# Performance work log

Hardware: AMD Instinct MI355X
Metric: run time of the kernel (lower is better)

## Reference

```python
import jax, jax.numpy as jnp
import numpy as np

N, E, F_IN, HID, G, HEADS = 50000, 300000, 128, 256, 1000, 1
NUM_GC, ALPHA = 5, 0.5
EPS_LN = 1e-5
EPS_BN = 1e-5


def _layer_norm(h, g, b):
    m = h.mean(-1, keepdims=True)
    v = jnp.mean((h - m) ** 2, axis=-1, keepdims=True)
    return (h - m) * jax.lax.rsqrt(v + EPS_LN) * g + b


def _l2_normalize_rows(h):
    # F.normalize(h, dim=1)
    n = jnp.sqrt(jnp.sum(h * h, axis=1, keepdims=True))
    return h / jnp.maximum(n, 1e-12)


def full_attention_conv(qs, ks, vs):
    # qs:[N,H,M] ks:[L,H,M] vs:[L,H,D]; global (Frobenius) norm as in torch.norm(p=2)
    qs = qs / jnp.linalg.norm(qs)
    ks = ks / jnp.linalg.norm(ks)
    n = qs.shape[0]
    kvs = jnp.einsum('lhm,lhd->hmd', ks, vs)                 # [H,M,D]
    attn_num = jnp.einsum('nhm,hmd->nhd', qs, kvs) + n * vs  # [N,H,D]
    ks_sum = ks.sum(axis=0)                                  # [H,M]
    norm = jnp.einsum('nhm,hm->nh', qs, ks_sum)[..., None] + n
    return attn_num / norm                                   # [N,H,D]


def setup_inputs() -> dict:
    key = jax.random.key(0)
    ks = jax.random.split(key, 24)
    f32 = jnp.float32

    def lin(k, fan_in, shape):
        return jax.random.normal(k, shape, f32) / np.sqrt(fan_in)

    inp = {}
    inp['x'] = jax.random.normal(ks[0], (N, F_IN), f32)
    inp['edge_index'] = jax.random.randint(ks[1], (2, E), 0, N)
    inp['batch'] = jnp.sort(jax.random.randint(ks[2], (N,), 0, G))
    inp['beta'] = 1
    # TransConv params
    inp['fc_W'] = lin(ks[3], F_IN, (F_IN, HID)); inp['fc_b'] = jnp.zeros((HID,), f32)
    inp['ln0_g'] = jnp.ones((HID,), f32); inp['ln0_b'] = jnp.zeros((HID,), f32)
    inp['Wq'] = lin(ks[4], HID, (HID, HID * HEADS)); inp['bq'] = jnp.zeros((HID * HEADS,), f32)
    inp['Wk'] = lin(ks[5], HID, (HID, HID * HEADS)); inp['bk'] = jnp.zeros((HID * HEADS,), f32)
    inp['Wv'] = lin(ks[6], HID, (HID, HID * HEADS)); inp['bv'] = jnp.zeros((HID * HEADS,), f32)
    inp['ln1_g'] = jnp.ones((HID,), f32); inp['ln1_b'] = jnp.zeros((HID,), f32)
    # GCN stack params
    inp['gcn_W0'] = lin(ks[7], F_IN, (F_IN, HID)); inp['gcn_b0'] = jnp.zeros((HID,), f32)
    inp['gcn_W'] = jnp.stack([lin(ks[8 + i], HID, (HID, HID)) for i in range(NUM_GC - 1)])
    inp['gcn_b'] = jnp.zeros((NUM_GC - 1, HID), f32)
    inp['bn_g'] = jnp.ones((NUM_GC, HID), f32); inp['bn_b'] = jnp.zeros((NUM_GC, HID), f32)
    inp['bn_mean'] = jnp.zeros((NUM_GC, HID), f32); inp['bn_var'] = jnp.ones((NUM_GC, HID), f32)
    return inp


def reference(x, edge_index, batch, beta, fc_W, fc_b, ln0_g, ln0_b,
              Wq, bq, Wk, bk, Wv, bv, ln1_g, ln1_b,
              gcn_W0, gcn_b0, gcn_W, gcn_b, bn_g, bn_b, bn_mean, bn_var):
    n = x.shape[0]
    # ---- TransConv branch (eval mode: dropout = identity) ----
    h = jax.nn.relu(_layer_norm(x @ fc_W + fc_b, ln0_g, ln0_b))
    qs = (h @ Wq + bq).reshape(n, HEADS, HID)
    kk = (h @ Wk + bk).reshape(n, HEADS, HID)
    vv = (h @ Wv + bv).reshape(n, HEADS, HID)
    attn = full_attention_conv(qs, kk, vv).mean(axis=1)      # [N,HID]
    h1 = ALPHA * attn + (1.0 - ALPHA) * h                    # residual
    h1 = jax.nn.relu(_layer_norm(h1, ln1_g, ln1_b))
    x_trans = _l2_normalize_rows(h1)
    # ---- GCN stack ----
    src, dst = edge_index[0], edge_index[1]
    loop = jnp.arange(n)
    src_f = jnp.concatenate([src, loop])
    dst_f = jnp.concatenate([dst, loop])
    deg = jax.ops.segment_sum(jnp.ones_like(src_f, dtype=x.dtype), dst_f, num_segments=n)
    dinv = jax.lax.rsqrt(deg)  # deg >= 1 due to self loops
    enorm = (dinv[src_f] * dinv[dst_f])[:, None]             # [E+N,1]
    g = x
    for i in range(NUM_GC):
        W = gcn_W0 if i == 0 else gcn_W[i - 1]
        b = gcn_b0 if i == 0 else gcn_b[i - 1]
        gw = g @ W
        g = jax.ops.segment_sum(gw[src_f] * enorm, dst_f, num_segments=n) + b
        g = (g - bn_mean[i]) * jax.lax.rsqrt(bn_var[i] + EPS_BN) * bn_g[i] + bn_b[i]
        if i != NUM_GC - 1:
            g = jax.nn.relu(g)
    g = _l2_normalize_rows(g)
    xpool = jax.ops.segment_sum(g, batch, num_segments=G)    # global_add_pool
    return (xpool, g, x_trans)
```

## Files before the change

kernel.cpp:

```cpp
#include <hip/hip_runtime.h>
#include <stdint.h>

#define NN 50000
#define NEDGE 300000
#define FIN 128
#define HID 256
#define NG 1000
#define NLAYER 5

typedef __bf16 bf16x8 __attribute__((ext_vector_type(8)));
typedef float f32x4 __attribute__((ext_vector_type(4)));

__device__ __forceinline__ float us2f(unsigned short u){
  union{ unsigned int i; float f; } c; c.i = ((unsigned int)u) << 16; return c.f;
}
__device__ __forceinline__ unsigned short f2us(float f){
  union{ float f; unsigned int i; } c; c.f = f;
  unsigned int r = c.i + 0x7fff + ((c.i >> 16) & 1);
  return (unsigned short)(r >> 16);
}

__device__ __forceinline__ void gload16(const void* g, void* l){
  __builtin_amdgcn_global_load_lds((__attribute__((address_space(1))) void*)g,
                                   (__attribute__((address_space(3))) void*)l, 16, 0, 0);
}

__device__ __forceinline__ void fma8(float* a, uint4 u, float w){
  a[0] += w * us2f((unsigned short)(u.x & 0xffff));
  a[1] += w * us2f((unsigned short)(u.x >> 16));
  a[2] += w * us2f((unsigned short)(u.y & 0xffff));
  a[3] += w * us2f((unsigned short)(u.y >> 16));
  a[4] += w * us2f((unsigned short)(u.z & 0xffff));
  a[5] += w * us2f((unsigned short)(u.z >> 16));
  a[6] += w * us2f((unsigned short)(u.w & 0xffff));
  a[7] += w * us2f((unsigned short)(u.w >> 16));
}

template<int K, int EPI>
__global__ void gemm_epi(const unsigned short* __restrict__ A,
                         const unsigned short* __restrict__ Wt,
                         const float* __restrict__ bias,
                         const float* __restrict__ p1,
                         const float* __restrict__ p2,
                         const unsigned short* __restrict__ hres,
                         void* __restrict__ outv, int nrows)
{
  __shared__ __align__(16) char smem[40960];
  unsigned short* Alds = (unsigned short*)smem;
  unsigned short* Wlds = (unsigned short*)(smem + 8192);
  const int t = threadIdx.x;
  const int lane = t & 63, w = t >> 6;
  const int r0 = blockIdx.x * 64;

  const int ccl = (t & 3) ^ ((t >> 3) & 3);
  int arow = r0 + (t >> 2); if (arow > nrows - 1) arow = nrows - 1;
  const unsigned short* aSrc = A + (size_t)arow * K + ccl * 8;
  const unsigned short* wSrc[4];
#pragma unroll
  for (int i = 0; i < 4; ++i){
    int c = i * 64 + (t >> 2);
    wSrc[i] = Wt + (size_t)c * K + ccl * 8;
  }

  f32x4 acc[4][4] = {};
  const int lg = lane >> 4, lr = lane & 15;

  for (int k0 = 0; k0 < K; k0 += 64){
    gload16(aSrc + k0,      smem + t * 16);
    gload16(aSrc + k0 + 32, smem + 4096 + t * 16);
#pragma unroll
    for (int i = 0; i < 4; ++i){
      gload16(wSrc[i] + k0,      smem + 8192  + (i * 256 + t) * 16);
      gload16(wSrc[i] + k0 + 32, smem + 24576 + (i * 256 + t) * 16);
    }
    __syncthreads();

#pragma unroll
    for (int kk = 0; kk < 2; ++kk){
      const unsigned short* Ak = Alds + kk * 2048;
      const unsigned short* Wk = Wlds + kk * 8192;
      bf16x8 af[4], bfr[4];
#pragma unroll
      for (int mi = 0; mi < 4; ++mi){
        int r = mi * 16 + lr;
        int cp = lg ^ ((r >> 1) & 3);
        af[mi] = *(const bf16x8*)(Ak + (r * 4 + cp) * 8);
      }
#pragma unroll
      for (int ni = 0; ni < 4; ++ni){
        int c = w * 64 + ni * 16 + lr;
        int cp = lg ^ ((c >> 1) & 3);
        bfr[ni] = *(const bf16x8*)(Wk + (c * 4 + cp) * 8);
      }
#pragma unroll
      for (int mi = 0; mi < 4; ++mi)
#pragma unroll
        for (int ni = 0; ni < 4; ++ni)
          acc[mi][ni] = __builtin_amdgcn_mfma_f32_16x16x32_bf16(af[mi], bfr[ni], acc[mi][ni], 0, 0, 0);
    }
    __syncthreads();
  }

  float g1[4], g2[4], bc[4];
#pragma unroll
  for (int ni = 0; ni < 4; ++ni){
    int c = w * 64 + ni * 16 + lr;
    g1[ni] = p1[c]; g2[ni] = p2[c];
    if (EPI <= 2) bc[ni] = bias[c];
  }

  float* redS = (float*)smem;
  float* redQ = redS + 256;
  float* meanr = redQ + 256;
  float* rstdr = meanr + 64;
  float* invr  = rstdr + 64;

  if (EPI == 1 || EPI == 2){
#pragma unroll
    for (int mi = 0; mi < 4; ++mi)
#pragma unroll
      for (int ni = 0; ni < 4; ++ni)
#pragma unroll
        for (int e = 0; e < 4; ++e){
          float v = acc[mi][ni][e] + bc[ni];
          if (EPI == 2){
            int gr = r0 + mi * 16 + lg * 4 + e; if (gr > nrows - 1) gr = nrows - 1;
            int c = w * 64 + ni * 16 + lr;
            v = 0.5f * v + 0.5f * us2f(hres[(size_t)gr * 256 + c]);
          }
          acc[mi][ni][e] = v;
        }
    float ps[4][4], pq[4][4];
#pragma unroll
    for (int mi = 0; mi < 4; ++mi)
#pragma unroll
      for (int e = 0; e < 4; ++e){
        float s = 0.f, q = 0.f;
#pragma unroll
        for (int ni = 0; ni < 4; ++ni){ float v = acc[mi][ni][e]; s += v; q += v * v; }
        ps[mi][e] = s; pq[mi][e] = q;
      }
#pragma unroll
    for (int m = 1; m <= 8; m <<= 1)
#pragma unroll
      for (int mi = 0; mi < 4; ++mi)
#pragma unroll
        for (int e = 0; e < 4; ++e){
          ps[mi][e] += __shfl_xor(ps[mi][e], m);
          pq[mi][e] += __shfl_xor(pq[mi][e], m);
        }
    if (lr == 0){
#pragma unroll
      for (int mi = 0; mi < 4; ++mi)
#pragma unroll
        for (int e = 0; e < 4; ++e){
          int row = mi * 16 + lg * 4 + e;
          redS[w * 64 + row] = ps[mi][e];
          redQ[w * 64 + row] = pq[mi][e];
        }
    }
    __syncthreads();
    if (t < 64){
      float S = redS[t] + redS[64 + t] + redS[128 + t] + redS[192 + t];
      float Q = redQ[t] + redQ[64 + t] + redQ[128 + t] + redQ[192 + t];
      float mean = S * (1.f / 256.f);
      float var = Q * (1.f / 256.f) - mean * mean;
      meanr[t] = mean; rstdr[t] = rsqrtf(var + 1e-5f);
    }
    __syncthreads();
#pragma unroll
    for (int mi = 0; mi < 4; ++mi)
#pragma unroll
      for (int e = 0; e < 4; ++e){
        int row = mi * 16 + lg * 4 + e;
        float mean = meanr[row], rstd = rstdr[row];
#pragma unroll
        for (int ni = 0; ni < 4; ++ni){
          float y = (acc[mi][ni][e] - mean) * rstd * g1[ni] + g2[ni];
          acc[mi][ni][e] = fmaxf(y, 0.f);
        }
      }
  } else {
#pragma unroll
    for (int mi = 0; mi < 4; ++mi)
#pragma unroll
      for (int ni = 0; ni < 4; ++ni)
#pragma unroll
        for (int e = 0; e < 4; ++e){
          float y = acc[mi][ni][e] * g1[ni] + g2[ni];
          if (EPI == 3) y = fmaxf(y, 0.f);
          acc[mi][ni][e] = y;
        }
  }

  if (EPI == 1 || EPI == 3){
    unsigned short* out = (unsigned short*)outv;
#pragma unroll
    for (int mi = 0; mi < 4; ++mi)
#pragma unroll
      for (int e = 0; e < 4; ++e){
        int gr = r0 + mi * 16 + lg * 4 + e;
        if (gr < nrows){
          unsigned short* orow = out + (size_t)gr * 256 + w * 64 + lr;
#pragma unroll
          for (int ni = 0; ni < 4; ++ni)
            orow[ni * 16] = f2us(acc[mi][ni][e]);
        }
      }
  } else {
    float ps[4][4];
#pragma unroll
    for (int mi = 0; mi < 4; ++mi)
#pragma unroll
      for (int e = 0; e < 4; ++e){
        float s = 0.f;
#pragma unroll
        for (int ni = 0; ni < 4; ++ni){ float v = acc[mi][ni][e]; s += v * v; }
        ps[mi][e] = s;
      }
#pragma unroll
    for (int m = 1; m <= 8; m <<= 1)
#pragma unroll
      for (int mi = 0; mi < 4; ++mi)
#pragma unroll
        for (int e = 0; e < 4; ++e)
          ps[mi][e] += __shfl_xor(ps[mi][e], m);
    __syncthreads();
    if (lr == 0){
#pragma unroll
      for (int mi = 0; mi < 4; ++mi)
#pragma unroll
        for (int e = 0; e < 4; ++e)
          redS[w * 64 + mi * 16 + lg * 4 + e] = ps[mi][e];
    }
    __syncthreads();
    if (t < 64){
      float S = redS[t] + redS[64 + t] + redS[128 + t] + redS[192 + t];
      invr[t] = 1.f / fmaxf(sqrtf(S), 1e-12f);
    }
    __syncthreads();
    float* out = (float*)outv;
#pragma unroll
    for (int mi = 0; mi < 4; ++mi)
#pragma unroll
      for (int e = 0; e < 4; ++e){
        int row = mi * 16 + lg * 4 + e;
        int gr = r0 + row;
        float inv = invr[row];
        if (gr < nrows){
          float* orow = out + (size_t)gr * 256 + w * 64 + lr;
#pragma unroll
          for (int ni = 0; ni < 4; ++ni)
            orow[ni * 16] = acc[mi][ni][e] * inv;
        }
      }
  }
}

#define PB_CVT 3125
#define PB_WP  112
#define PB_BN  NLAYER
#define PB_GB  196
#define PB_DC  1172
#define PB_TOTAL (PB_CVT + PB_WP + PB_BN + PB_GB + PB_DC)

__global__ void k_pre(const float* __restrict__ x, unsigned short* __restrict__ xb,
                      const float* __restrict__ fcW, const float* __restrict__ Wv,
                      const float* __restrict__ gW0, const float* __restrict__ gW,
                      unsigned short* __restrict__ fcWt, unsigned short* __restrict__ WvT,
                      unsigned short* __restrict__ g0T, unsigned short* __restrict__ gWT,
                      const float* __restrict__ gb0, const float* __restrict__ gb,
                      const float* __restrict__ bng, const float* __restrict__ bnb,
                      const float* __restrict__ bnm, const float* __restrict__ bnv,
                      float* __restrict__ bnscale, float* __restrict__ bnshift,
                      const int* __restrict__ batch, int* __restrict__ gstart,
                      const int* __restrict__ ei, int* __restrict__ deg)
{
  __shared__ unsigned short tile[64][65];
  int b = blockIdx.x, t = threadIdx.x;
  if (b < PB_CVT){
    int i = b * 256 + t;
    const float4* sp = (const float4*)x + (size_t)i * 2;
    float4 a = sp[0], bb = sp[1];
    ushort4 u0, u1;
    u0.x = f2us(a.x); u0.y = f2us(a.y); u0.z = f2us(a.z); u0.w = f2us(a.w);
    u1.x = f2us(bb.x); u1.y = f2us(bb.y); u1.z = f2us(bb.z); u1.w = f2us(bb.w);
    ushort4* dp = (ushort4*)xb + (size_t)i * 2;
    dp[0] = u0; dp[1] = u1;
    return;
  }
  b -= PB_CVT;
  if (b < PB_WP){
    int which = b >> 4, r = b & 15;
    const float* src; unsigned short* dst; int K;
    if (which == 0){ src = fcW; dst = fcWt; K = FIN; }
    else if (which == 1){ src = Wv; dst = WvT; K = 256; }
    else if (which == 2){ src = gW0; dst = g0T; K = FIN; }
    else { src = gW + (size_t)(which - 3) * 65536; dst = gWT + (size_t)(which - 3) * 65536; K = 256; }
    int bx = (r & 3) * 64; if (bx >= K) return;
    int by = (r >> 2) * 64;
#pragma unroll
    for (int j = 0; j < 16; ++j){
      int idx = j * 256 + t;
      int rr = idx >> 6, cc = idx & 63;
      tile[rr][cc] = f2us(src[(size_t)(bx + rr) * 256 + by + cc]);
    }
    __syncthreads();
#pragma unroll
    for (int j = 0; j < 16; ++j){
      int idx = j * 256 + t;
      int rr = idx >> 6, cc = idx & 63;
      dst[(size_t)(by + rr) * K + bx + cc] = tile[cc][rr];
    }
    return;
  }
  b -= PB_WP;
  if (b < PB_BN){
    int i = b * 256 + t;
    float bias = (b == 0) ? gb0[t] : gb[(b - 1) * 256 + t];
    float sc = bng[i] * rsqrtf(bnv[i] + 1e-5f);
    bnscale[i] = sc;
    bnshift[i] = (bias - bnm[i]) * sc + bnb[i];
    return;
  }
  b -= PB_BN;
  if (b < PB_GB){
    int i = b * 256 + t;
    if (i >= NN) return;
    int bc = batch[i];
    int bp = (i == 0) ? -1 : batch[i - 1];
    for (int g = bp + 1; g <= bc; ++g) gstart[g] = i;
    if (i == NN - 1)
      for (int g = bc + 1; g <= NG; ++g) gstart[g] = NN;
    return;
  }
  b -= PB_GB;
  {
    int e = b * 256 + t;
    if (e < NEDGE) atomicAdd(&deg[ei[NEDGE + e]], 1);
  }
}

__global__ void k_scan_part(const int* __restrict__ deg, int* rp, int* bsum){
  __shared__ int sh[256];
  int t = threadIdx.x, i = blockIdx.x * 256 + t;
  int v = (i < NN) ? deg[i] + 1 : 0;
  sh[t] = v; __syncthreads();
  for (int off = 1; off < 256; off <<= 1){
    int x = (t >= off) ? sh[t - off] : 0;
    __syncthreads(); sh[t] += x; __syncthreads();
  }
  if (i < NN) rp[i] = sh[t] - v;
  if (t == 255) bsum[blockIdx.x] = sh[255];
}
__global__ void k_scan_sums(int* rp, int* bsum, int nb){
  __shared__ int sh[256];
  int t = threadIdx.x;
  int v = (t < nb) ? bsum[t] : 0;
  sh[t] = v; __syncthreads();
  for (int off = 1; off < 256; off <<= 1){
    int x = (t >= off) ? sh[t - off] : 0;
    __syncthreads(); sh[t] += x; __syncthreads();
  }
  if (t < nb) bsum[t] = sh[t] - v;
  if (t == 0) rp[NN] = sh[255];
}
__global__ void k_scan_add(int* rp, const int* __restrict__ bsum, const int* __restrict__ deg,
                           int* fill, float* dinv){
  int i = blockIdx.x * 256 + threadIdx.x;
  if (i < NN){
    int r = rp[i] + bsum[i >> 8];
    rp[i] = r; fill[i] = r;
    dinv[i] = rsqrtf((float)(deg[i] + 1));
  }
}

__global__ void k_fill(const int* __restrict__ ei, int* __restrict__ fill,
                       int* __restrict__ colx, float* __restrict__ ew,
                       const float* __restrict__ dinv)
{
  int e = blockIdx.x * 256 + threadIdx.x;
  if (e < NEDGE){
    int s = ei[e], d = ei[NEDGE + e];
    int p = atomicAdd(&fill[d], 1);
    colx[p] = s; ew[p] = dinv[s] * dinv[d];
  } else if (e < NEDGE + NN){
    int i = e - NEDGE;
    int p = atomicAdd(&fill[i], 1);
    float di = dinv[i];
    colx[p] = i; ew[p] = di * di;
  }
}

template<int NC>
__global__ void __launch_bounds__(256) k_aggregate(
    const unsigned short* __restrict__ gsrc, const int* __restrict__ rp,
    const int* __restrict__ colx, const float* __restrict__ ew,
    unsigned short* __restrict__ gout)
{
  constexpr int LG = (NC == 256) ? 5 : 4;
  int tid = blockIdx.x * 256 + threadIdx.x;
  int nd = tid >> LG;
  if (nd >= NN) return;
  int c0 = (tid & ((1 << LG) - 1)) * 8;
  const unsigned short* base = gsrc + c0;
  int jb = rp[nd], je = rp[nd + 1];
  float a0[8] = {}, a1[8] = {};
  int j = jb;
  for (; j + 2 <= je; j += 2){
    int s0 = colx[j], s1 = colx[j + 1];
    float w0 = ew[j], w1 = ew[j + 1];
    uint4 u0 = *(const uint4*)(base + (size_t)s0 * NC);
    uint4 u1 = *(const uint4*)(base + (size_t)s1 * NC);
    fma8(a0, u0, w0);
    fma8(a1, u1, w1);
  }
  if (j < je){
    uint4 u = *(const uint4*)(base + (size_t)colx[j] * NC);
    fma8(a0, u, ew[j]);
  }
  uint4 pk;
  pk.x = (unsigned int)f2us(a0[0] + a1[0]) | ((unsigned int)f2us(a0[1] + a1[1]) << 16);
  pk.y = (unsigned int)f2us(a0[2] + a1[2]) | ((unsigned int)f2us(a0[3] + a1[3]) << 16);
  pk.z = (unsigned int)f2us(a0[4] + a1[4]) | ((unsigned int)f2us(a0[5] + a1[5]) << 16);
  pk.w = (unsigned int)f2us(a0[6] + a1[6]) | ((unsigned int)f2us(a0[7] + a1[7]) << 16);
  *(uint4*)(gout + (size_t)nd * NC + c0) = pk;
}

__global__ void k_pool(const float* __restrict__ out1, const int* __restrict__ gstart,
                       float* __restrict__ out0)
{
  int g = blockIdx.x, c = threadIdx.x;
  int js = gstart[g], je = gstart[g + 1];
  float acc = 0.f;
  int r = js;
  for (; r + 4 <= je; r += 4){
    float a = out1[(size_t)r * 256 + c];
    float b = out1[(size_t)(r + 1) * 256 + c];
    float d = out1[(size_t)(r + 2) * 256 + c];
    float e = out1[(size_t)(r + 3) * 256 + c];
    acc += (a + b) + (d + e);
  }
  for (; r < je; ++r) acc += out1[(size_t)r * 256 + c];
  out0[(size_t)g * 256 + c] = acc;
}

extern "C" void kernel_launch(void* const* d_in, const int* in_sizes, int n_in,
                              void* d_out, int out_size, void* d_ws, size_t ws_size,
                              hipStream_t stream)
{
  const float* x    = (const float*)d_in[0];
  const int*  ei    = (const int*)d_in[1];
  const int*  batch = (const int*)d_in[2];
  const float* fcW  = (const float*)d_in[4];
  const float* fcb  = (const float*)d_in[5];
  const float* ln0g = (const float*)d_in[6];
  const float* ln0b = (const float*)d_in[7];
  const float* Wv   = (const float*)d_in[12];
  const float* bv   = (const float*)d_in[13];
  const float* ln1g = (const float*)d_in[14];
  const float* ln1b = (const float*)d_in[15];
  const float* gW0  = (const float*)d_in[16];
  const float* gb0  = (const float*)d_in[17];
  const float* gW   = (const float*)d_in[18];
  const float* gb   = (const float*)d_in[19];
  const float* bng  = (const float*)d_in[20];
  const float* bnb  = (const float*)d_in[21];
  const float* bnm  = (const float*)d_in[22];
  const float* bnv  = (const float*)d_in[23];

  char* ws = (char*)d_ws;
  unsigned short* xb   = (unsigned short*)(ws);
  unsigned short* hb   = (unsigned short*)(ws + 12800000);
  unsigned short* ga   = (unsigned short*)(ws + 38400000);
  unsigned short* fcWt = (unsigned short*)(ws + 64000000);
  unsigned short* WvT  = (unsigned short*)(ws + 64065536);
  unsigned short* g0T  = (unsigned short*)(ws + 64196608);
  unsigned short* gWT  = (unsigned short*)(ws + 64262144);
  float* bnscale       = (float*)(ws + 64786432);
  float* bnshift       = (float*)(ws + 64791552);
  int*   deg           = (int*)(ws + 64796672);
  int*   rp            = (int*)(ws + 64996672);
  int*   fill          = (int*)(ws + 65196736);
  float* dinv          = (float*)(ws + 65396736);
  int*   colx          = (int*)(ws + 65596736);
  float* ew            = (float*)(ws + 66996736);
  int*   bsum          = (int*)(ws + 68396736);
  int*   gstart        = (int*)(ws + 68397760);

  float* out0 = (float*)d_out;
  float* out1 = out0 + NG * 256;
  float* out2 = out1 + NN * 256;

  hipMemsetAsync(deg, 0, NN * sizeof(int), stream);
  k_pre<<<PB_TOTAL, 256, 0, stream>>>(x, xb, fcW, Wv, gW0, gW, fcWt, WvT, g0T, gWT,
                                      gb0, gb, bng, bnb, bnm, bnv, bnscale, bnshift,
                                      batch, gstart, ei, deg);
  k_scan_part<<<196, 256, 0, stream>>>(deg, rp, bsum);
  k_scan_sums<<<1, 256, 0, stream>>>(rp, bsum, 196);
  k_scan_add<<<196, 256, 0, stream>>>(rp, bsum, deg, fill, dinv);
  k_fill<<<(NEDGE + NN + 255) / 256, 256, 0, stream>>>(ei, fill, colx, ew, dinv);

  const int GB = (NN + 63) / 64;
  gemm_epi<FIN, 1><<<GB, 256, 0, stream>>>(xb, fcWt, fcb, ln0g, ln0b, nullptr, hb, NN);
  gemm_epi<256, 2><<<GB, 256, 0, stream>>>(hb, WvT, bv, ln1g, ln1b, hb, out2, NN);

  const int AB128 = (NN * 16 + 255) / 256;
  const int AB256 = (NN * 32 + 255) / 256;
  k_aggregate<128><<<AB128, 256, 0, stream>>>(xb, rp, colx, ew, ga);
  gemm_epi<FIN, 3><<<GB, 256, 0, stream>>>(ga, g0T, nullptr, bnscale, bnshift, nullptr, hb, NN);
  for (int i = 1; i < NLAYER - 1; ++i){
    k_aggregate<256><<<AB256, 256, 0, stream>>>(hb, rp, colx, ew, ga);
    gemm_epi<256, 3><<<GB, 256, 0, stream>>>(ga, gWT + (size_t)(i - 1) * 65536, nullptr,
        bnscale + i * 256, bnshift + i * 256, nullptr, hb, NN);
  }
  k_aggregate<256><<<AB256, 256, 0, stream>>>(hb, rp, colx, ew, ga);
  gemm_epi<256, 4><<<GB, 256, 0, stream>>>(ga, gWT + (size_t)3 * 65536, nullptr,
      bnscale + 4 * 256, bnshift + 4 * 256, nullptr, out1, NN);

  k_pool<<<NG, 256, 0, stream>>>(out1, gstart, out0);
}
```

Baseline: 339.4 us.

## Double-buffer GEMM LDS tiles with async prefetch and unroll aggregation by four

Result: no change. 345.3 us (+1.7%).

```diff
diff --git a/kernel.cpp b/kernel.cpp
--- a/kernel.cpp
+++ b/kernel.cpp
@@ -46,8 +46,6 @@
                          void* __restrict__ outv, int nrows)
 {
   __shared__ __align__(16) char smem[40960];
-  unsigned short* Alds = (unsigned short*)smem;
-  unsigned short* Wlds = (unsigned short*)(smem + 8192);
   const int t = threadIdx.x;
   const int lane = t & 63, w = t >> 6;
   const int r0 = blockIdx.x * 64;
@@ -64,41 +62,55 @@
 
   f32x4 acc[4][4] = {};
   const int lg = lane >> 4, lr = lane & 15;
-
-  for (int k0 = 0; k0 < K; k0 += 64){
-    gload16(aSrc + k0,      smem + t * 16);
-    gload16(aSrc + k0 + 32, smem + 4096 + t * 16);
-#pragma unroll
-    for (int i = 0; i < 4; ++i){
-      gload16(wSrc[i] + k0,      smem + 8192  + (i * 256 + t) * 16);
-      gload16(wSrc[i] + k0 + 32, smem + 24576 + (i * 256 + t) * 16);
-    }
-    __syncthreads();
-
-#pragma unroll
-    for (int kk = 0; kk < 2; ++kk){
-      const unsigned short* Ak = Alds + kk * 2048;
-      const unsigned short* Wk = Wlds + kk * 8192;
-      bf16x8 af[4], bfr[4];
-#pragma unroll
-      for (int mi = 0; mi < 4; ++mi){
-        int r = mi * 16 + lr;
-        int cp = lg ^ ((r >> 1) & 3);
-        af[mi] = *(const bf16x8*)(Ak + (r * 4 + cp) * 8);
-      }
-#pragma unroll
-      for (int ni = 0; ni < 4; ++ni){
-        int c = w * 64 + ni * 16 + lr;
-        int cp = lg ^ ((c >> 1) & 3);
-        bfr[ni] = *(const bf16x8*)(Wk + (c * 4 + cp) * 8);
-      }
-#pragma unroll
-      for (int mi = 0; mi < 4; ++mi)
-#pragma unroll
-        for (int ni = 0; ni < 4; ++ni)
-          acc[mi][ni] = __builtin_amdgcn_mfma_f32_16x16x32_bf16(af[mi], bfr[ni], acc[mi][ni], 0, 0, 0);
-    }
-    __syncthreads();
+  constexpr int NIT = K / 32;
+
+  gload16(aSrc, smem + t * 16);
+#pragma unroll
+  for (int i = 0; i < 4; ++i)
+    gload16(wSrc[i], smem + 4096 + (i * 256 + t) * 16);
+
+#pragma unroll
+  for (int it = 0; it < NIT; ++it){
+    const int cur = it & 1;
+    if (it + 1 < NIT){
+      const int nxt = (it + 1) & 1;
+      const int k1 = (it + 1) * 32;
+      gload16(aSrc + k1, smem + nxt * 20480 + t * 16);
+#pragma unroll
+      for (int i = 0; i < 4; ++i)
+        gload16(wSrc[i] + k1, smem + nxt * 20480 + 4096 + (i * 256 + t) * 16);
+      asm volatile("s_waitcnt vmcnt(5)" ::: "memory");
+    } else {
+      asm volatile("s_waitcnt vmcnt(0)" ::: "memory");
+    }
+    __builtin_amdgcn_sched_barrier(0);
+    __builtin_amdgcn_s_barrier();
+    __builtin_amdgcn_sched_barrier(0);
+
+    const unsigned short* Ak = (const unsigned short*)(smem + cur * 20480);
+    const unsigned short* Wk = (const unsigned short*)(smem + cur * 20480 + 4096);
+    bf16x8 af[4], bfr[4];
+#pragma unroll
+    for (int mi = 0; mi < 4; ++mi){
+      int r = mi * 16 + lr;
+      int cp = lg ^ ((r >> 1) & 3);
+      af[mi] = *(const bf16x8*)(Ak + (r * 4 + cp) * 8);
+    }
+#pragma unroll
+    for (int ni = 0; ni < 4; ++ni){
+      int c = w * 64 + ni * 16 + lr;
+      int cp = lg ^ ((c >> 1) & 3);
+      bfr[ni] = *(const bf16x8*)(Wk + (c * 4 + cp) * 8);
+    }
+#pragma unroll
+    for (int mi = 0; mi < 4; ++mi)
+#pragma unroll
+      for (int ni = 0; ni < 4; ++ni)
+        acc[mi][ni] = __builtin_amdgcn_mfma_f32_16x16x32_bf16(af[mi], bfr[ni], acc[mi][ni], 0, 0, 0);
+
+    __builtin_amdgcn_sched_barrier(0);
+    __builtin_amdgcn_s_barrier();
+    __builtin_amdgcn_sched_barrier(0);
   }
 
   float g1[4], g2[4], bc[4];
@@ -407,13 +419,22 @@
   int jb = rp[nd], je = rp[nd + 1];
   float a0[8] = {}, a1[8] = {};
   int j = jb;
+  for (; j + 4 <= je; j += 4){
+    int s0 = colx[j], s1 = colx[j + 1], s2 = colx[j + 2], s3 = colx[j + 3];
+    float w0 = ew[j], w1 = ew[j + 1], w2 = ew[j + 2], w3 = ew[j + 3];
+    uint4 u0 = *(const uint4*)(base + (size_t)s0 * NC);
+    uint4 u1 = *(const uint4*)(base + (size_t)s1 * NC);
+    uint4 u2 = *(const uint4*)(base + (size_t)s2 * NC);
+    uint4 u3 = *(const uint4*)(base + (size_t)s3 * NC);
+    fma8(a0, u0, w0); fma8(a1, u1, w1);
+    fma8(a0, u2, w2); fma8(a1, u3, w3);
+  }
   for (; j + 2 <= je; j += 2){
     int s0 = colx[j], s1 = colx[j + 1];
     float w0 = ew[j], w1 = ew[j + 1];
     uint4 u0 = *(const uint4*)(base + (size_t)s0 * NC);
     uint4 u1 = *(const uint4*)(base + (size_t)s1 * NC);
-    fma8(a0, u0, w0);
-    fma8(a1, u1, w1);
+    fma8(a0, u0, w0); fma8(a1, u1, w1);
   }
   if (j < je){
     uint4 u = *(const uint4*)(base + (size_t)colx[j] * NC);
```

## Fuse sparse neighbor aggregation into GCN GEMM via LDS-staged gathered A tile

Applied to the files above, without the earlier changes.

Result: slower. 463.8 us (+36.7%).

```diff
diff --git a/kernel.cpp b/kernel.cpp
--- a/kernel.cpp
+++ b/kernel.cpp
@@ -106,7 +106,7 @@
   for (int ni = 0; ni < 4; ++ni){
     int c = w * 64 + ni * 16 + lr;
     g1[ni] = p1[c]; g2[ni] = p2[c];
-    if (EPI <= 2) bc[ni] = bias[c];
+    bc[ni] = bias[c];
   }
 
   float* redS = (float*)smem;
@@ -115,85 +115,72 @@
   float* rstdr = meanr + 64;
   float* invr  = rstdr + 64;
 
-  if (EPI == 1 || EPI == 2){
-#pragma unroll
-    for (int mi = 0; mi < 4; ++mi)
-#pragma unroll
-      for (int ni = 0; ni < 4; ++ni)
-#pragma unroll
-        for (int e = 0; e < 4; ++e){
-          float v = acc[mi][ni][e] + bc[ni];
-          if (EPI == 2){
-            int gr = r0 + mi * 16 + lg * 4 + e; if (gr > nrows - 1) gr = nrows - 1;
-            int c = w * 64 + ni * 16 + lr;
-            v = 0.5f * v + 0.5f * us2f(hres[(size_t)gr * 256 + c]);
-          }
-          acc[mi][ni][e] = v;
+#pragma unroll
+  for (int mi = 0; mi < 4; ++mi)
+#pragma unroll
+    for (int ni = 0; ni < 4; ++ni)
+#pragma unroll
+      for (int e = 0; e < 4; ++e){
+        float v = acc[mi][ni][e] + bc[ni];
+        if (EPI == 2){
+          int gr = r0 + mi * 16 + lg * 4 + e; if (gr > nrows - 1) gr = nrows - 1;
+          int c = w * 64 + ni * 16 + lr;
+          v = 0.5f * v + 0.5f * us2f(hres[(size_t)gr * 256 + c]);
         }
-    float ps[4][4], pq[4][4];
-#pragma unroll
-    for (int mi = 0; mi < 4; ++mi)
-#pragma unroll
-      for (int e = 0; e < 4; ++e){
-        float s = 0.f, q = 0.f;
-#pragma unroll
-        for (int ni = 0; ni < 4; ++ni){ float v = acc[mi][ni][e]; s += v; q += v * v; }
-        ps[mi][e] = s; pq[mi][e] = q;
-      }
-#pragma unroll
-    for (int m = 1; m <= 8; m <<= 1)
-#pragma unroll
-      for (int mi = 0; mi < 4; ++mi)
-#pragma unroll
-        for (int e = 0; e < 4; ++e){
-          ps[mi][e] += __shfl_xor(ps[mi][e], m);
-          pq[mi][e] += __shfl_xor(pq[mi][e], m);
-        }
-    if (lr == 0){
-#pragma unroll
-      for (int mi = 0; mi < 4; ++mi)
-#pragma unroll
-        for (int e = 0; e < 4; ++e){
-          int row = mi * 16 + lg * 4 + e;
-          redS[w * 64 + row] = ps[mi][e];
-          redQ[w * 64 + row] = pq[mi][e];
-        }
-    }
-    __syncthreads();
-    if (t < 64){
-      float S = redS[t] + redS[64 + t] + redS[128 + t] + redS[192 + t];
-      float Q = redQ[t] + redQ[64 + t] + redQ[128 + t] + redQ[192 + t];
-      float mean = S * (1.f / 256.f);
-      float var = Q * (1.f / 256.f) - mean * mean;
-      meanr[t] = mean; rstdr[t] = rsqrtf(var + 1e-5f);
-    }
-    __syncthreads();
+        acc[mi][ni][e] = v;
+      }
+  float ps[4][4], pq[4][4];
+#pragma unroll
+  for (int mi = 0; mi < 4; ++mi)
+#pragma unroll
+    for (int e = 0; e < 4; ++e){
+      float s = 0.f, q = 0.f;
+#pragma unroll
+      for (int ni = 0; ni < 4; ++ni){ float v = acc[mi][ni][e]; s += v; q += v * v; }
+      ps[mi][e] = s; pq[mi][e] = q;
+    }
+#pragma unroll
+  for (int m = 1; m <= 8; m <<= 1)
+#pragma unroll
+    for (int mi = 0; mi < 4; ++mi)
+#pragma unroll
+      for (int e = 0; e < 4; ++e){
+        ps[mi][e] += __shfl_xor(ps[mi][e], m);
+        pq[mi][e] += __shfl_xor(pq[mi][e], m);
+      }
+  if (lr == 0){
 #pragma unroll
     for (int mi = 0; mi < 4; ++mi)
 #pragma unroll
       for (int e = 0; e < 4; ++e){
         int row = mi * 16 + lg * 4 + e;
-        float mean = meanr[row], rstd = rstdr[row];
-#pragma unroll
-        for (int ni = 0; ni < 4; ++ni){
-          float y = (acc[mi][ni][e] - mean) * rstd * g1[ni] + g2[ni];
-          acc[mi][ni][e] = fmaxf(y, 0.f);
-        }
-      }
-  } else {
-#pragma unroll
-    for (int mi = 0; mi < 4; ++mi)
-#pragma unroll
-      for (int ni = 0; ni < 4; ++ni)
-#pragma unroll
-        for (int e = 0; e < 4; ++e){
-          float y = acc[mi][ni][e] * g1[ni] + g2[ni];
-          if (EPI == 3) y = fmaxf(y, 0.f);
-          acc[mi][ni][e] = y;
-        }
-  }
-
-  if (EPI == 1 || EPI == 3){
+        redS[w * 64 + row] = ps[mi][e];
+        redQ[w * 64 + row] = pq[mi][e];
+      }
+  }
+  __syncthreads();
+  if (t < 64){
+    float S = redS[t] + redS[64 + t] + redS[128 + t] + redS[192 + t];
+    float Q = redQ[t] + redQ[64 + t] + redQ[128 + t] + redQ[192 + t];
+    float mean = S * (1.f / 256.f);
+    float var = Q * (1.f / 256.f) - mean * mean;
+    meanr[t] = mean; rstdr[t] = rsqrtf(var + 1e-5f);
+  }
+  __syncthreads();
+#pragma unroll
+  for (int mi = 0; mi < 4; ++mi)
+#pragma unroll
+    for (int e = 0; e < 4; ++e){
+      int row = mi * 16 + lg * 4 + e;
+      float mean = meanr[row], rstd = rstdr[row];
+#pragma unroll
+      for (int ni = 0; ni < 4; ++ni){
+        float y = (acc[mi][ni][e] - mean) * rstd * g1[ni] + g2[ni];
+        acc[mi][ni][e] = fmaxf(y, 0.f);
+      }
+    }
+
+  if (EPI == 1){
     unsigned short* out = (unsigned short*)outv;
 #pragma unroll
     for (int mi = 0; mi < 4; ++mi)
@@ -208,6 +195,182 @@
         }
       }
   } else {
+    float ps2[4][4];
+#pragma unroll
+    for (int mi = 0; mi < 4; ++mi)
+#pragma unroll
+      for (int e = 0; e < 4; ++e){
+        float s = 0.f;
+#pragma unroll
+        for (int ni = 0; ni < 4; ++ni){ float v = acc[mi][ni][e]; s += v * v; }
+        ps2[mi][e] = s;
+      }
+#pragma unroll
+    for (int m = 1; m <= 8; m <<= 1)
+#pragma unroll
+      for (int mi = 0; mi < 4; ++mi)
+#pragma unroll
+        for (int e = 0; e < 4; ++e)
+          ps2[mi][e] += __shfl_xor(ps2[mi][e], m);
+    __syncthreads();
+    if (lr == 0){
+#pragma unroll
+      for (int mi = 0; mi < 4; ++mi)
+#pragma unroll
+        for (int e = 0; e < 4; ++e)
+          redS[w * 64 + mi * 16 + lg * 4 + e] = ps2[mi][e];
+    }
+    __syncthreads();
+    if (t < 64){
+      float S = redS[t] + redS[64 + t] + redS[128 + t] + redS[192 + t];
+      invr[t] = 1.f / fmaxf(sqrtf(S), 1e-12f);
+    }
+    __syncthreads();
+    float* out = (float*)outv;
+#pragma unroll
+    for (int mi = 0; mi < 4; ++mi)
+#pragma unroll
+      for (int e = 0; e < 4; ++e){
+        int row = mi * 16 + lg * 4 + e;
+        int gr = r0 + row;
+        float inv = invr[row];
+        if (gr < nrows){
+          float* orow = out + (size_t)gr * 256 + w * 64 + lr;
+#pragma unroll
+          for (int ni = 0; ni < 4; ++ni)
+            orow[ni * 16] = acc[mi][ni][e] * inv;
+        }
+      }
+  }
+}
+
+template<int K, int EPI>
+__global__ void __launch_bounds__(256) gemm_gather_epi(
+    const unsigned short* __restrict__ Asrc,
+    const unsigned short* __restrict__ Wt,
+    const float* __restrict__ p1, const float* __restrict__ p2,
+    const int* __restrict__ rp, const int* __restrict__ colx,
+    const float* __restrict__ ew,
+    void* __restrict__ outv, int nrows)
+{
+  constexpr int ABYTES = 64 * K * 2;
+  __shared__ __align__(16) char smem[ABYTES + 16384];
+  unsigned short* Alds = (unsigned short*)smem;
+  char* Wsm = smem + ABYTES;
+  const int t = threadIdx.x;
+  const int lane = t & 63, w = t >> 6;
+  const int r0 = blockIdx.x * 64;
+
+  constexpr int NCG = K / 8;
+  constexpr int NSL = 64 * NCG / 256;
+  constexpr int NDSH = (K == 256) ? 5 : 4;
+#pragma unroll
+  for (int s = 0; s < NSL; ++s){
+    int slice = t + s * 256;
+    int nd = slice >> NDSH;
+    int cg = slice & (NCG - 1);
+    int gr = r0 + nd;
+    int jb = 0, je = 0;
+    if (gr < nrows){ jb = rp[gr]; je = rp[gr + 1]; }
+    const unsigned short* base = Asrc + cg * 8;
+    float a0[8] = {}, a1[8] = {};
+    int j = jb;
+    for (; j + 2 <= je; j += 2){
+      int s0 = colx[j], s1 = colx[j + 1];
+      float w0 = ew[j], w1 = ew[j + 1];
+      uint4 u0 = *(const uint4*)(base + (size_t)s0 * K);
+      uint4 u1 = *(const uint4*)(base + (size_t)s1 * K);
+      fma8(a0, u0, w0); fma8(a1, u1, w1);
+    }
+    if (j < je){
+      uint4 u = *(const uint4*)(base + (size_t)colx[j] * K);
+      fma8(a0, u, ew[j]);
+    }
+    uint4 pk;
+    pk.x = (unsigned int)f2us(a0[0] + a1[0]) | ((unsigned int)f2us(a0[1] + a1[1]) << 16);
+    pk.y = (unsigned int)f2us(a0[2] + a1[2]) | ((unsigned int)f2us(a0[3] + a1[3]) << 16);
+    pk.z = (unsigned int)f2us(a0[4] + a1[4]) | ((unsigned int)f2us(a0[5] + a1[5]) << 16);
+    pk.w = (unsigned int)f2us(a0[6] + a1[6]) | ((unsigned int)f2us(a0[7] + a1[7]) << 16);
+    int addr = (cg >> 2) * 2048 + nd * 32 + (((cg & 3) ^ ((nd >> 1) & 3)) * 8);
+    *(uint4*)(Alds + addr) = pk;
+  }
+
+  const int ccl = (t & 3) ^ ((t >> 3) & 3);
+  const unsigned short* wSrc[4];
+#pragma unroll
+  for (int i = 0; i < 4; ++i){
+    int c = i * 64 + (t >> 2);
+    wSrc[i] = Wt + (size_t)c * K + ccl * 8;
+  }
+  f32x4 acc[4][4] = {};
+  const int lg = lane >> 4, lr = lane & 15;
+
+  __syncthreads();
+
+  for (int k0 = 0; k0 < K; k0 += 32){
+    if (k0) __syncthreads();
+#pragma unroll
+    for (int i = 0; i < 4; ++i)
+      gload16(wSrc[i] + k0, Wsm + (i * 256 + t) * 16);
+    __syncthreads();
+
+    const unsigned short* Ak = Alds + (k0 >> 5) * 2048;
+    const unsigned short* Wk = (const unsigned short*)Wsm;
+    bf16x8 af[4], bfr[4];
+#pragma unroll
+    for (int mi = 0; mi < 4; ++mi){
+      int r = mi * 16 + lr;
+      int cp = lg ^ ((r >> 1) & 3);
+      af[mi] = *(const bf16x8*)(Ak + (r * 4 + cp) * 8);
+    }
+#pragma unroll
+    for (int ni = 0; ni < 4; ++ni){
+      int c = w * 64 + ni * 16 + lr;
+      int cp = lg ^ ((c >> 1) & 3);
+      bfr[ni] = *(const bf16x8*)(Wk + (c * 4 + cp) * 8);
+    }
+#pragma unroll
+    for (int mi = 0; mi < 4; ++mi)
+#pragma unroll
+      for (int ni = 0; ni < 4; ++ni)
+        acc[mi][ni] = __builtin_amdgcn_mfma_f32_16x16x32_bf16(af[mi], bfr[ni], acc[mi][ni], 0, 0, 0);
+  }
+  __syncthreads();
+
+  float g1[4], g2[4];
+#pragma unroll
+  for (int ni = 0; ni < 4; ++ni){
+    int c = w * 64 + ni * 16 + lr;
+    g1[ni] = p1[c]; g2[ni] = p2[c];
+  }
+#pragma unroll
+  for (int mi = 0; mi < 4; ++mi)
+#pragma unroll
+    for (int ni = 0; ni < 4; ++ni)
+#pragma unroll
+      for (int e = 0; e < 4; ++e){
+        float y = acc[mi][ni][e] * g1[ni] + g2[ni];
+        if (EPI == 3) y = fmaxf(y, 0.f);
+        acc[mi][ni][e] = y;
+      }
+
+  if (EPI == 3){
+    unsigned short* out = (unsigned short*)outv;
+#pragma unroll
+    for (int mi = 0; mi < 4; ++mi)
+#pragma unroll
+      for (int e = 0; e < 4; ++e){
+        int gr = r0 + mi * 16 + lg * 4 + e;
+        if (gr < nrows){
+          unsigned short* orow = out + (size_t)gr * 256 + w * 64 + lr;
+#pragma unroll
+          for (int ni = 0; ni < 4; ++ni)
+            orow[ni * 16] = f2us(acc[mi][ni][e]);
+        }
+      }
+  } else {
+    float* redS = (float*)smem;
+    float* invr = redS + 256;
     float ps[4][4];
 #pragma unroll
     for (int mi = 0; mi < 4; ++mi)
@@ -225,7 +388,6 @@
 #pragma unroll
         for (int e = 0; e < 4; ++e)
           ps[mi][e] += __shfl_xor(ps[mi][e], m);
-    __syncthreads();
     if (lr == 0){
 #pragma unroll
       for (int mi = 0; mi < 4; ++mi)
@@ -392,41 +554,6 @@
   }
 }
 
-template<int NC>
-__global__ void __launch_bounds__(256) k_aggregate(
-    const unsigned short* __restrict__ gsrc, const int* __restrict__ rp,
-    const int* __restrict__ colx, const float* __restrict__ ew,
-    unsigned short* __restrict__ gout)
-{
-  constexpr int LG = (NC == 256) ? 5 : 4;
-  int tid = blockIdx.x * 256 + threadIdx.x;
-  int nd = tid >> LG;
-  if (nd >= NN) return;
-  int c0 = (tid & ((1 << LG) - 1)) * 8;
-  const unsigned short* base = gsrc + c0;
-  int jb = rp[nd], je = rp[nd + 1];
-  float a0[8] = {}, a1[8] = {};
-  int j = jb;
-  for (; j + 2 <= je; j += 2){
-    int s0 = colx[j], s1 = colx[j + 1];
-    float w0 = ew[j], w1 = ew[j + 1];
-    uint4 u0 = *(const uint4*)(base + (size_t)s0 * NC);
-    uint4 u1 = *(const uint4*)(base + (size_t)s1 * NC);
-    fma8(a0, u0, w0);
-    fma8(a1, u1, w1);
-  }
-  if (j < je){
-    uint4 u = *(const uint4*)(base + (size_t)colx[j] * NC);
-    fma8(a0, u, ew[j]);
-  }
-  uint4 pk;
-  pk.x = (unsigned int)f2us(a0[0] + a1[0]) | ((unsigned int)f2us(a0[1] + a1[1]) << 16);
-  pk.y = (unsigned int)f2us(a0[2] + a1[2]) | ((unsigned int)f2us(a0[3] + a1[3]) << 16);
-  pk.z = (unsigned int)f2us(a0[4] + a1[4]) | ((unsigned int)f2us(a0[5] + a1[5]) << 16);
-  pk.w = (unsigned int)f2us(a0[6] + a1[6]) | ((unsigned int)f2us(a0[7] + a1[7]) << 16);
-  *(uint4*)(gout + (size_t)nd * NC + c0) = pk;
-}
-
 __global__ void k_pool(const float* __restrict__ out1, const int* __restrict__ gstart,
                        float* __restrict__ out0)
 {
@@ -472,7 +599,7 @@
   char* ws = (char*)d_ws;
   unsigned short* xb   = (unsigned short*)(ws);
   unsigned short* hb   = (unsigned short*)(ws + 12800000);
-  unsigned short* ga   = (unsigned short*)(ws + 38400000);
+  unsigned short* hb2  = (unsigned short*)(ws + 38400000);
   unsigned short* fcWt = (unsigned short*)(ws + 64000000);
   unsigned short* WvT  = (unsigned short*)(ws + 64065536);
   unsigned short* g0T  = (unsigned short*)(ws + 64196608);
@@ -505,18 +632,16 @@
   gemm_epi<FIN, 1><<<GB, 256, 0, stream>>>(xb, fcWt, fcb, ln0g, ln0b, nullptr, hb, NN);
   gemm_epi<256, 2><<<GB, 256, 0, stream>>>(hb, WvT, bv, ln1g, ln1b, hb, out2, NN);
 
-  const int AB128 = (NN * 16 + 255) / 256;
-  const int AB256 = (NN * 32 + 255) / 256;
-  k_aggregate<128><<<AB128, 256, 0, stream>>>(xb, rp, colx, ew, ga);
-  gemm_epi<FIN, 3><<<GB, 256, 0, stream>>>(ga, g0T, nullptr, bnscale, bnshift, nullptr, hb, NN);
-  for (int i = 1; i < NLAYER - 1; ++i){
-    k_aggregate<256><<<AB256, 256, 0, stream>>>(hb, rp, colx, ew, ga);
-    gemm_epi<256, 3><<<GB, 256, 0, stream>>>(ga, gWT + (size_t)(i - 1) * 65536, nullptr,
-        bnscale + i * 256, bnshift + i * 256, nullptr, hb, NN);
-  }
-  k_aggregate<256><<<AB256, 256, 0, stream>>>(hb, rp, colx, ew, ga);
-  gemm_epi<256, 4><<<GB, 256, 0, stream>>>(ga, gWT + (size_t)3 * 65536, nullptr,
-      bnscale + 4 * 256, bnshift + 4 * 256, nullptr, out1, NN);
+  gemm_gather_epi<FIN, 3><<<GB, 256, 0, stream>>>(xb, g0T, bnscale, bnshift,
+      rp, colx, ew, hb, NN);
+  gemm_gather_epi<256, 3><<<GB, 256, 0, stream>>>(hb, gWT + 0 * 65536,
+      bnscale + 1 * 256, bnshift + 1 * 256, rp, colx, ew, hb2, NN);
+  gemm_gather_epi<256, 3><<<GB, 256, 0, stream>>>(hb2, gWT + 1 * 65536,
+      bnscale + 2 * 256, bnshift + 2 * 256, rp, colx, ew, hb, NN);
+  gemm_gather_epi<256, 3><<<GB, 256, 0, stream>>>(hb, gWT + 2 * 65536,
+      bnscale + 3 * 256, bnshift + 3 * 256, rp, colx, ew, hb2, NN);
+  gemm_gather_epi<256, 4><<<GB, 256, 0, stream>>>(hb2, gWT + 3 * 65536,
+      bnscale + 4 * 256, bnshift + 4 * 256, rp, colx, ew, out1, NN);
 
   k_pool<<<NG, 256, 0, stream>>>(out1, gstart, out0);
 }
```
